# Kernel tuning notes

Hardware: AMD Instinct MI355X
Metric: run time of the kernel (lower is better)

The kernel has to match this reference:

```python
import jax, jax.numpy as jnp
import numpy as np


def setup_inputs() -> dict:
    key = jax.random.key(0)
    kx, ky = jax.random.split(key)
    B, N, D = 16, 2048, 128
    x = jax.random.normal(kx, (B, N, D), dtype=jnp.float32)
    y = jax.random.normal(ky, (B, N, D), dtype=jnp.float32)
    return {"x": x, "y": y}


def reference(x, y):
    # Pairwise squared-Euclidean cost: out[b, i, j] = sum_d (x[b,i,d] - y[b,j,d])**2
    # Computed via ||x||^2 + ||y||^2 - 2 <x, y> to avoid the O(N^2 D) intermediate
    # that the original repeat/view pattern materializes.
    x2 = jnp.sum(x * x, axis=-1)                      # [B, N]
    y2 = jnp.sum(y * y, axis=-1)                      # [B, N]
    xy = jnp.einsum('bid,bjd->bij', x, y)             # [B, N, N]
    cost = x2[:, :, None] + y2[:, None, :] - 2.0 * xy  # [B, N, N]
    return jnp.maximum(cost, 0.0)
```

## Files before the change

### kernel.cpp

```cpp
#include <hip/hip_runtime.h>


#define Bb   16
#define Nn   2048
#define Dd   128
#define TILE 128
#define LDSS 136

typedef __bf16 bf16x8 __attribute__((ext_vector_type(8)));
typedef float  f32x4  __attribute__((ext_vector_type(4)));

__device__ __forceinline__ unsigned int f2bf(float f) {
  unsigned int u = __float_as_uint(f);
  return (u + 0x7FFFu + ((u >> 16) & 1u)) >> 16;
}

__global__ __launch_bounds__(256, 2)
void pairwise_cost_kernel(const float* __restrict__ x,
                          const float* __restrict__ y,
                          float* __restrict__ out) {
  __shared__ __align__(16) unsigned short xs[TILE * LDSS];
  __shared__ __align__(16) unsigned short ys[TILE * LDSS];
  __shared__ float xn_s[TILE];
  __shared__ float yn_s[TILE];

  const int t  = threadIdx.x;
  const int b  = blockIdx.z;
  const int i0 = blockIdx.y * TILE;
  const int j0 = blockIdx.x * TILE;

  const int r    = t >> 1;
  const int half = t & 1;

  {
    const float4* src = (const float4*)(x + ((size_t)b * Nn + (i0 + r)) * Dd + half * 64);
    float ss = 0.f;
    #pragma unroll
    for (int q = 0; q < 8; ++q) {
      float4 v0 = src[2 * q];
      float4 v1 = src[2 * q + 1];
      ss += v0.x * v0.x + v0.y * v0.y + v0.z * v0.z + v0.w * v0.w
          + v1.x * v1.x + v1.y * v1.y + v1.z * v1.z + v1.w * v1.w;
      uint4 pk;
      pk.x = f2bf(v0.x) | (f2bf(v0.y) << 16);
      pk.y = f2bf(v0.z) | (f2bf(v0.w) << 16);
      pk.z = f2bf(v1.x) | (f2bf(v1.y) << 16);
      pk.w = f2bf(v1.z) | (f2bf(v1.w) << 16);
      *(uint4*)&xs[r * LDSS + half * 64 + q * 8] = pk;
    }
    ss += __shfl_xor(ss, 1);
    if (half == 0) xn_s[r] = ss;
  }
  {
    const float4* src = (const float4*)(y + ((size_t)b * Nn + (j0 + r)) * Dd + half * 64);
    float ss = 0.f;
    #pragma unroll
    for (int q = 0; q < 8; ++q) {
      float4 v0 = src[2 * q];
      float4 v1 = src[2 * q + 1];
      ss += v0.x * v0.x + v0.y * v0.y + v0.z * v0.z + v0.w * v0.w
          + v1.x * v1.x + v1.y * v1.y + v1.z * v1.z + v1.w * v1.w;
      uint4 pk;
      pk.x = f2bf(v0.x) | (f2bf(v0.y) << 16);
      pk.y = f2bf(v0.z) | (f2bf(v0.w) << 16);
      pk.z = f2bf(v1.x) | (f2bf(v1.y) << 16);
      pk.w = f2bf(v1.z) | (f2bf(v1.w) << 16);
      *(uint4*)&ys[r * LDSS + half * 64 + q * 8] = pk;
    }
    ss += __shfl_xor(ss, 1);
    if (half == 0) yn_s[r] = ss;
  }
  __syncthreads();

  const int w    = t >> 6;
  const int lane = t & 63;
  const int lrow = lane & 15;
  const int quad = lane >> 4;
  const int wr   = (w >> 1) * 64;
  const int wc   = (w & 1) * 64;

  f32x4 acc[4][4];
  #pragma unroll
  for (int i = 0; i < 4; ++i)
    #pragma unroll
    for (int j = 0; j < 4; ++j)
      acc[i][j] = (f32x4){0.f, 0.f, 0.f, 0.f};

  #pragma unroll
  for (int k = 0; k < 4; ++k) {
    const int dk = k * 32 + quad * 8;
    bf16x8 af[4], bfr[4];
    #pragma unroll
    for (int ti = 0; ti < 4; ++ti)
      af[ti] = *(const bf16x8*)&xs[(wr + ti * 16 + lrow) * LDSS + dk];
    #pragma unroll
    for (int tj = 0; tj < 4; ++tj)
      bfr[tj] = *(const bf16x8*)&ys[(wc + tj * 16 + lrow) * LDSS + dk];
    #pragma unroll
    for (int ti = 0; ti < 4; ++ti)
      #pragma unroll
      for (int tj = 0; tj < 4; ++tj)
        acc[ti][tj] = __builtin_amdgcn_mfma_f32_16x16x32_bf16(af[ti], bfr[tj], acc[ti][tj], 0, 0, 0);
  }

  float* outb = out + (size_t)b * Nn * Nn;
  #pragma unroll
  for (int ti = 0; ti < 4; ++ti) {
    float xn[4];
    #pragma unroll
    for (int rg = 0; rg < 4; ++rg)
      xn[rg] = xn_s[wr + ti * 16 + quad * 4 + rg];
    #pragma unroll
    for (int tj = 0; tj < 4; ++tj) {
      const float yn = yn_s[wc + tj * 16 + lrow];
      const int   jj = j0 + wc + tj * 16 + lrow;
      #pragma unroll
      for (int rg = 0; rg < 4; ++rg) {
        const int ii  = i0 + wr + ti * 16 + quad * 4 + rg;
        float cval    = xn[rg] + yn - 2.0f * acc[ti][tj][rg];
        outb[(size_t)ii * Nn + jj] = fmaxf(cval, 0.0f);
      }
    }
  }
}

extern "C" void kernel_launch(void* const* d_in, const int* in_sizes, int n_in,
                              void* d_out, int out_size, void* d_ws, size_t ws_size,
                              hipStream_t stream) {
  const float* x = (const float*)d_in[0];
  const float* y = (const float*)d_in[1];
  float* out = (float*)d_out;
  dim3 grid(Nn / TILE, Nn / TILE, Bb);
  pairwise_cost_kernel<<<grid, dim3(256, 1, 1), 0, stream>>>(x, y, out);
}
```

Measured before the change: 356.0 us.

## Keep x fragments in registers and loop over double-buffered y tiles per block

Each block now handles eight consecutive 128-column y tiles. The x fragments and norms stay in registers for the whole loop, and the next y tile is prefetched into a second LDS buffer while the current tile runs through MFMA. MFMA operands are swapped so each lane holds four consecutive output columns, which allows 16-byte vector stores instead of scalar ones. This cuts redundant x loads and conversions and improves store coalescing. In exchange it raises register pressure from the prefetch buffer and the x fragments, and the grid becomes 8x smaller, which may underfill the GPU.

```diff
diff --git a/kernel.cpp b/kernel.cpp
--- a/kernel.cpp
+++ b/kernel.cpp
@@ -5,35 +5,65 @@
 #define Nn   2048
 #define Dd   128
 #define TILE 128
+#define JT   8
 #define LDSS 136
 
 typedef __bf16 bf16x8 __attribute__((ext_vector_type(8)));
 typedef float  f32x4  __attribute__((ext_vector_type(4)));
 
-__device__ __forceinline__ unsigned int f2bf(float f) {
-  unsigned int u = __float_as_uint(f);
-  return (u + 0x7FFFu + ((u >> 16) & 1u)) >> 16;
+__device__ __forceinline__ bf16x8 pack8(float4 a, float4 b) {
+  bf16x8 r;
+  r[0] = (__bf16)a.x; r[1] = (__bf16)a.y; r[2] = (__bf16)a.z; r[3] = (__bf16)a.w;
+  r[4] = (__bf16)b.x; r[5] = (__bf16)b.y; r[6] = (__bf16)b.z; r[7] = (__bf16)b.w;
+  return r;
 }
 
 __global__ __launch_bounds__(256, 2)
 void pairwise_cost_kernel(const float* __restrict__ x,
                           const float* __restrict__ y,
                           float* __restrict__ out) {
-  __shared__ __align__(16) unsigned short xs[TILE * LDSS];
-  __shared__ __align__(16) unsigned short ys[TILE * LDSS];
-  __shared__ float xn_s[TILE];
-  __shared__ float yn_s[TILE];
+  __shared__ __align__(16) unsigned short ys[2][TILE * LDSS];
+  __shared__ __align__(16) float          yn_s[2][TILE];
 
   const int t  = threadIdx.x;
   const int b  = blockIdx.z;
   const int i0 = blockIdx.y * TILE;
-  const int j0 = blockIdx.x * TILE;
+  const int j0 = blockIdx.x * (TILE * JT);
+
+  const int w    = t >> 6;
+  const int lane = t & 63;
+  const int lrow = lane & 15;
+  const int quad = lane >> 4;
+  const int ib   = (w >> 1) * 64;
+  const int jb   = (w & 1) * 64;
 
   const int r    = t >> 1;
   const int half = t & 1;
 
+  bf16x8 xf[4][4];
+  float  xn[4];
   {
-    const float4* src = (const float4*)(x + ((size_t)b * Nn + (i0 + r)) * Dd + half * 64);
+    const float* xb = x + ((size_t)b * Nn + i0 + ib) * Dd;
+    #pragma unroll
+    for (int ti = 0; ti < 4; ++ti) {
+      const float* rp = xb + (ti * 16 + lrow) * Dd + quad * 8;
+      float ss = 0.f;
+      #pragma unroll
+      for (int k = 0; k < 4; ++k) {
+        float4 u0 = *(const float4*)(rp + k * 32);
+        float4 u1 = *(const float4*)(rp + k * 32 + 4);
+        ss += u0.x * u0.x + u0.y * u0.y + u0.z * u0.z + u0.w * u0.w
+            + u1.x * u1.x + u1.y * u1.y + u1.z * u1.z + u1.w * u1.w;
+        xf[ti][k] = pack8(u0, u1);
+      }
+      ss += __shfl_xor(ss, 16);
+      ss += __shfl_xor(ss, 32);
+      xn[ti] = ss;
+    }
+  }
+
+  {
+    const float4* src = (const float4*)(y + ((size_t)b * Nn + j0 + r) * Dd + half * 64);
     float ss = 0.f;
     #pragma unroll
     for (int q = 0; q < 8; ++q) {
@@ -41,86 +71,79 @@
       float4 v1 = src[2 * q + 1];
       ss += v0.x * v0.x + v0.y * v0.y + v0.z * v0.z + v0.w * v0.w
           + v1.x * v1.x + v1.y * v1.y + v1.z * v1.z + v1.w * v1.w;
-      uint4 pk;
-      pk.x = f2bf(v0.x) | (f2bf(v0.y) << 16);
-      pk.y = f2bf(v0.z) | (f2bf(v0.w) << 16);
-      pk.z = f2bf(v1.x) | (f2bf(v1.y) << 16);
-      pk.w = f2bf(v1.z) | (f2bf(v1.w) << 16);
-      *(uint4*)&xs[r * LDSS + half * 64 + q * 8] = pk;
+      *(bf16x8*)&ys[0][r * LDSS + half * 64 + q * 8] = pack8(v0, v1);
     }
     ss += __shfl_xor(ss, 1);
-    if (half == 0) xn_s[r] = ss;
-  }
-  {
-    const float4* src = (const float4*)(y + ((size_t)b * Nn + (j0 + r)) * Dd + half * 64);
-    float ss = 0.f;
-    #pragma unroll
-    for (int q = 0; q < 8; ++q) {
-      float4 v0 = src[2 * q];
-      float4 v1 = src[2 * q + 1];
-      ss += v0.x * v0.x + v0.y * v0.y + v0.z * v0.z + v0.w * v0.w
-          + v1.x * v1.x + v1.y * v1.y + v1.z * v1.z + v1.w * v1.w;
-      uint4 pk;
-      pk.x = f2bf(v0.x) | (f2bf(v0.y) << 16);
-      pk.y = f2bf(v0.z) | (f2bf(v0.w) << 16);
-      pk.z = f2bf(v1.x) | (f2bf(v1.y) << 16);
-      pk.w = f2bf(v1.z) | (f2bf(v1.w) << 16);
-      *(uint4*)&ys[r * LDSS + half * 64 + q * 8] = pk;
-    }
-    ss += __shfl_xor(ss, 1);
-    if (half == 0) yn_s[r] = ss;
+    if (half == 0) yn_s[0][r] = ss;
   }
   __syncthreads();
 
-  const int w    = t >> 6;
-  const int lane = t & 63;
-  const int lrow = lane & 15;
-  const int quad = lane >> 4;
-  const int wr   = (w >> 1) * 64;
-  const int wc   = (w & 1) * 64;
+  float* outb = out + (size_t)b * Nn * Nn;
 
-  f32x4 acc[4][4];
-  #pragma unroll
-  for (int i = 0; i < 4; ++i)
-    #pragma unroll
-    for (int j = 0; j < 4; ++j)
-      acc[i][j] = (f32x4){0.f, 0.f, 0.f, 0.f};
+  for (int jt = 0; jt < JT; ++jt) {
+    const int cur = jt & 1;
 
-  #pragma unroll
-  for (int k = 0; k < 4; ++k) {
-    const int dk = k * 32 + quad * 8;
-    bf16x8 af[4], bfr[4];
-    #pragma unroll
-    for (int ti = 0; ti < 4; ++ti)
-      af[ti] = *(const bf16x8*)&xs[(wr + ti * 16 + lrow) * LDSS + dk];
-    #pragma unroll
-    for (int tj = 0; tj < 4; ++tj)
-      bfr[tj] = *(const bf16x8*)&ys[(wc + tj * 16 + lrow) * LDSS + dk];
+    float4 ld[16];
+    if (jt + 1 < JT) {
+      const float4* src =
+          (const float4*)(y + ((size_t)b * Nn + j0 + (jt + 1) * TILE + r) * Dd + half * 64);
+      #pragma unroll
+      for (int q = 0; q < 16; ++q) ld[q] = src[q];
+    }
+
+    f32x4 acc[4][4];
     #pragma unroll
     for (int ti = 0; ti < 4; ++ti)
       #pragma unroll
       for (int tj = 0; tj < 4; ++tj)
-        acc[ti][tj] = __builtin_amdgcn_mfma_f32_16x16x32_bf16(af[ti], bfr[tj], acc[ti][tj], 0, 0, 0);
-  }
+        acc[ti][tj] = (f32x4){0.f, 0.f, 0.f, 0.f};
 
-  float* outb = out + (size_t)b * Nn * Nn;
-  #pragma unroll
-  for (int ti = 0; ti < 4; ++ti) {
-    float xn[4];
     #pragma unroll
-    for (int rg = 0; rg < 4; ++rg)
-      xn[rg] = xn_s[wr + ti * 16 + quad * 4 + rg];
+    for (int k = 0; k < 4; ++k) {
+      const int dk = k * 32 + quad * 8;
+      bf16x8 yf[4];
+      #pragma unroll
+      for (int tj = 0; tj < 4; ++tj)
+        yf[tj] = *(const bf16x8*)&ys[cur][(jb + tj * 16 + lrow) * LDSS + dk];
+      #pragma unroll
+      for (int ti = 0; ti < 4; ++ti)
+        #pragma unroll
+        for (int tj = 0; tj < 4; ++tj)
+          acc[ti][tj] = __builtin_amdgcn_mfma_f32_16x16x32_bf16(yf[tj], xf[ti][k],
+                                                               acc[ti][tj], 0, 0, 0);
+    }
+
+    if (jt + 1 < JT) {
+      float ss = 0.f;
+      #pragma unroll
+      for (int q = 0; q < 8; ++q) {
+        float4 v0 = ld[2 * q];
+        float4 v1 = ld[2 * q + 1];
+        ss += v0.x * v0.x + v0.y * v0.y + v0.z * v0.z + v0.w * v0.w
+            + v1.x * v1.x + v1.y * v1.y + v1.z * v1.z + v1.w * v1.w;
+        *(bf16x8*)&ys[cur ^ 1][r * LDSS + half * 64 + q * 8] = pack8(v0, v1);
+      }
+      ss += __shfl_xor(ss, 1);
+      if (half == 0) yn_s[cur ^ 1][r] = ss;
+    }
+
     #pragma unroll
-    for (int tj = 0; tj < 4; ++tj) {
-      const float yn = yn_s[wc + tj * 16 + lrow];
-      const int   jj = j0 + wc + tj * 16 + lrow;
+    for (int ti = 0; ti < 4; ++ti) {
+      const size_t orow = (size_t)(i0 + ib + ti * 16 + lrow) * Nn + (j0 + jt * TILE + jb);
+      const float  xnv  = xn[ti];
       #pragma unroll
-      for (int rg = 0; rg < 4; ++rg) {
-        const int ii  = i0 + wr + ti * 16 + quad * 4 + rg;
-        float cval    = xn[rg] + yn - 2.0f * acc[ti][tj][rg];
-        outb[(size_t)ii * Nn + jj] = fmaxf(cval, 0.0f);
+      for (int tj = 0; tj < 4; ++tj) {
+        f32x4 yn4 = *(const f32x4*)&yn_s[cur][jb + tj * 16 + quad * 4];
+        f32x4 a   = acc[ti][tj];
+        f32x4 c;
+        #pragma unroll
+        for (int rg = 0; rg < 4; ++rg)
+          c[rg] = fmaxf(xnv + yn4[rg] - 2.0f * a[rg], 0.0f);
+        *(f32x4*)(outb + orow + tj * 16 + quad * 4) = c;
       }
     }
+
+    __syncthreads();
   }
 }
 
@@ -130,6 +153,6 @@
   const float* x = (const float*)d_in[0];
   const float* y = (const float*)d_in[1];
   float* out = (float*)d_out;
-  dim3 grid(Nn / TILE, Nn / TILE, Bb);
+  dim3 grid(Nn / (TILE * JT), Nn / TILE, Bb);
   pairwise_cost_kernel<<<grid, dim3(256, 1, 1), 0, stream>>>(x, y, out);
 }
```

New measurement: 371.9 us. 1.04x slower.
